# Performance work log

Hardware: AMD Instinct MI355X
Metric: run time of the kernel (lower is better)

Reference implementation:

```python
import jax, jax.numpy as jnp
import numpy as np

D_MODEL = 1024
NUM_HEADS = 16
D_K = D_MODEL // NUM_HEADS
BATCH = 4
SEQ = 2048


def setup_inputs() -> dict:
    key = jax.random.key(0)
    ks = jax.random.split(key, 16)
    s = 0.02
    return {
        "query": jax.random.normal(ks[0], (BATCH, SEQ, D_MODEL), jnp.float32),
        "key": jax.random.normal(ks[1], (BATCH, SEQ, D_MODEL), jnp.float32),
        "value": jax.random.normal(ks[2], (BATCH, SEQ, D_MODEL), jnp.float32),
        "Wq": jax.random.normal(ks[3], (D_MODEL, D_MODEL), jnp.float32) * s,
        "bq": jnp.zeros((D_MODEL,), jnp.float32),
        "Wk": jax.random.normal(ks[4], (D_MODEL, D_MODEL), jnp.float32) * s,
        "bk": jnp.zeros((D_MODEL,), jnp.float32),
        "Wv": jax.random.normal(ks[5], (D_MODEL, D_MODEL), jnp.float32) * s,
        "bv": jnp.zeros((D_MODEL,), jnp.float32),
        "Wo": jax.random.normal(ks[6], (D_MODEL, D_MODEL), jnp.float32) * s,
        "bo": jnp.zeros((D_MODEL,), jnp.float32),
        "gamma": jnp.ones((D_MODEL,), jnp.float32),
        "beta": jnp.zeros((D_MODEL,), jnp.float32),
    }


def _layer_norm(x, gamma, beta, eps=1e-5):
    mu = jnp.mean(x, axis=-1, keepdims=True)
    var = jnp.var(x, axis=-1, keepdims=True)
    return (x - mu) * jax.lax.rsqrt(var + eps) * gamma + beta


def reference(query, key, value, Wq, bq, Wk, bk, Wv, bv, Wo, bo, gamma, beta):
    B, S, _ = query.shape
    residual = query
    # projections -> [B, H, S, d_k]
    Q = (query @ Wq + bq).reshape(B, S, NUM_HEADS, D_K).transpose(0, 2, 1, 3)
    K = (key @ Wk + bk).reshape(B, -1, NUM_HEADS, D_K).transpose(0, 2, 1, 3)
    V = (value @ Wv + bv).reshape(B, -1, NUM_HEADS, D_K).transpose(0, 2, 1, 3)
    scale = 1.0 / jnp.sqrt(jnp.asarray(D_K, query.dtype))
    scores = jnp.einsum("bhqd,bhkd->bhqk", Q, K) * scale  # [B,H,S,S]
    attn = jax.nn.softmax(scores, axis=-1)
    ctx = jnp.einsum("bhqk,bhkd->bhqd", attn, V)
    ctx = ctx.transpose(0, 2, 1, 3).reshape(B, S, D_MODEL)
    out = ctx @ Wo + bo
    return _layer_norm(residual + out, gamma, beta)
```

## Files before the change

kernel.cpp:

```cpp
#include <hip/hip_runtime.h>

#define D_MODEL 1024
#define NUM_HEADS 16
#define DK 64
#define BATCH 4
#define SEQ 2048
#define MTOT (BATCH*SEQ)

typedef __attribute__((ext_vector_type(8))) short short8;
typedef __attribute__((ext_vector_type(4))) float f32x4;
typedef __attribute__((ext_vector_type(4))) unsigned int u32x4;

__device__ __forceinline__ unsigned short f2bf(float f) {
    union { float f; unsigned u; } v; v.f = f;
    unsigned r = v.u + 0x7FFFu + ((v.u >> 16) & 1u);
    return (unsigned short)(r >> 16);
}

__device__ __forceinline__ unsigned cvtpk(float lo, float hi) {
    unsigned r;
    asm("v_cvt_pk_bf16_f32 %0, %1, %2" : "=v"(r) : "v"(lo), "v"(hi));
    return r;
}

__device__ __forceinline__ void gload16(const unsigned short* g, unsigned short* l) {
    __builtin_amdgcn_global_load_lds(
        (const __attribute__((address_space(1))) unsigned int*)g,
        (__attribute__((address_space(3))) unsigned int*)l, 16, 0, 0);
}

__global__ __launch_bounds__(256) void mha_wtrans4(
    const float* __restrict__ W0, const float* __restrict__ W1,
    const float* __restrict__ W2, const float* __restrict__ W3,
    unsigned short* __restrict__ T0, unsigned short* __restrict__ T1,
    unsigned short* __restrict__ T2, unsigned short* __restrict__ T3) {
    __shared__ float tile[64][65];
    int z = blockIdx.z;
    const float* W = z == 0 ? W0 : z == 1 ? W1 : z == 2 ? W2 : W3;
    unsigned short* WT = z == 0 ? T0 : z == 1 ? T1 : z == 2 ? T2 : T3;
    int n0 = blockIdx.x * 64, k0 = blockIdx.y * 64;
    int tx = threadIdx.x & 63, ty = threadIdx.x >> 6;
#pragma unroll
    for (int i = 0; i < 16; ++i)
        tile[ty + i * 4][tx] = W[(size_t)(k0 + ty + i * 4) * D_MODEL + n0 + tx];
    __syncthreads();
#pragma unroll
    for (int i = 0; i < 16; ++i)
        WT[(size_t)(n0 + ty + i * 4) * D_MODEL + k0 + tx] = f2bf(tile[tx][ty + i * 4]);
}

__global__ __launch_bounds__(256) void mha_cvt3(
    const float* __restrict__ i0, const float* __restrict__ i1, const float* __restrict__ i2,
    unsigned short* __restrict__ o0, unsigned short* __restrict__ o1, unsigned short* __restrict__ o2) {
    int y = blockIdx.y;
    const float* in = y == 0 ? i0 : y == 1 ? i1 : i2;
    unsigned short* out = y == 0 ? o0 : y == 1 ? o1 : o2;
    int i = blockIdx.x * 256 + threadIdx.x;
    float4 v = reinterpret_cast<const float4*>(in)[i];
    ushort4 o;
    o.x = f2bf(v.x); o.y = f2bf(v.y); o.z = f2bf(v.z); o.w = f2bf(v.w);
    reinterpret_cast<ushort4*>(out)[i] = o;
}

__device__ __forceinline__ void gemm_stage(const unsigned short* Ag, const unsigned short* Bg,
                                           unsigned short* Al, unsigned short* Bl,
                                           int wid, int rsub, int c8, int kk,
                                           int brow, int bcol) {
#pragma unroll
    for (int q = 0; q < 4; ++q) {
        int i = wid * 4 + q;
        int row = i * 8 + rsub;
        int gcol = kk + ((c8 ^ (row & 7)) << 3);
        gload16(Ag + (size_t)(brow + row) * D_MODEL + gcol, Al + i * 512);
        gload16(Bg + (size_t)(bcol + row) * D_MODEL + gcol, Bl + i * 512);
    }
}

__device__ __forceinline__ void gemm_compute(const unsigned short* Al, const unsigned short* Bl,
                                             f32x4 (&acc)[4][4],
                                             int wr, int wc, int l15, int lg, int l7) {
    short8 af[4][2], bf[4][2];
#pragma unroll
    for (int mi = 0; mi < 4; ++mi)
#pragma unroll
        for (int ks = 0; ks < 2; ++ks)
            af[mi][ks] = *reinterpret_cast<const short8*>(
                &Al[(wr * 64 + mi * 16 + l15) * 64 + (((ks * 4 + lg) ^ l7) << 3)]);
#pragma unroll
    for (int ni = 0; ni < 4; ++ni)
#pragma unroll
        for (int ks = 0; ks < 2; ++ks)
            bf[ni][ks] = *reinterpret_cast<const short8*>(
                &Bl[(wc * 64 + ni * 16 + l15) * 64 + (((ks * 4 + lg) ^ l7) << 3)]);
#pragma unroll
    for (int mi = 0; mi < 4; ++mi)
#pragma unroll
        for (int ni = 0; ni < 4; ++ni)
#pragma unroll
            for (int ks = 0; ks < 2; ++ks)
                acc[mi][ni] = __builtin_amdgcn_mfma_f32_16x16x32_bf16(
                    af[mi][ks], bf[ni][ks], acc[mi][ni], 0, 0, 0);
}

__global__ __launch_bounds__(256) void mha_gemm_qkv(
    const unsigned short* __restrict__ Aq, const unsigned short* __restrict__ Ak,
    const unsigned short* __restrict__ Av,
    const unsigned short* __restrict__ Wq, const unsigned short* __restrict__ Wk,
    const unsigned short* __restrict__ Wv,
    const float* __restrict__ bq, const float* __restrict__ bk, const float* __restrict__ bv,
    unsigned short* __restrict__ Qb, unsigned short* __restrict__ Kb,
    unsigned short* __restrict__ VT, float qscale) {
    __shared__ unsigned short SM[32768];
    unsigned short* A0 = SM;
    unsigned short* B0 = SM + 8192;
    unsigned short* A1 = SM + 16384;
    unsigned short* B1 = SM + 24576;

    int z = blockIdx.z;
    const unsigned short* A = z == 0 ? Aq : z == 1 ? Ak : Av;
    const unsigned short* WT = z == 0 ? Wq : z == 1 ? Wk : Wv;
    const float* bias = z == 0 ? bq : z == 1 ? bk : bv;

    int wid = threadIdx.x >> 6;
    int lane = threadIdx.x & 63;
    int wr = wid >> 1, wc = wid & 1;
    int brow = blockIdx.x * 128;
    int bcol = blockIdx.y * 128;
    int l15 = lane & 15, lg = lane >> 4;
    int c8 = lane & 7, rsub = lane >> 3;
    int l7 = l15 & 7;

    f32x4 acc[4][4] = {};
    gemm_stage(A, WT, A0, B0, wid, rsub, c8, 0, brow, bcol);
    __syncthreads();
    for (int kk = 0; kk < D_MODEL; kk += 128) {
        gemm_stage(A, WT, A1, B1, wid, rsub, c8, kk + 64, brow, bcol);
        gemm_compute(A0, B0, acc, wr, wc, l15, lg, l7);
        __syncthreads();
        if (kk + 128 < D_MODEL)
            gemm_stage(A, WT, A0, B0, wid, rsub, c8, kk + 128, brow, bcol);
        gemm_compute(A1, B1, acc, wr, wc, l15, lg, l7);
        __syncthreads();
    }

    if (z < 2) {
        unsigned short* outb = z == 0 ? Qb : Kb;
        float scale = z == 0 ? qscale : 1.0f;
#pragma unroll
        for (int ni = 0; ni < 4; ++ni) {
            int col = bcol + wc * 64 + ni * 16 + l15;
            float bv2 = bias[col];
#pragma unroll
            for (int mi = 0; mi < 4; ++mi)
#pragma unroll
                for (int j = 0; j < 4; ++j) {
                    int row = brow + wr * 64 + mi * 16 + lg * 4 + j;
                    outb[(size_t)row * D_MODEL + col] = f2bf((acc[mi][ni][j] + bv2) * scale);
                }
        }
    } else {
        unsigned short* T = SM;
#pragma unroll
        for (int ni = 0; ni < 4; ++ni) {
            int c = wc * 64 + ni * 16 + l15;
            float bv2 = bias[bcol + c];
#pragma unroll
            for (int mi = 0; mi < 4; ++mi)
#pragma unroll
                for (int j = 0; j < 4; ++j) {
                    int r = wr * 64 + mi * 16 + lg * 4 + j;
                    T[c * 136 + r] = f2bf(acc[mi][ni][j] + bv2);
                }
        }
        __syncthreads();
        int c = threadIdx.x >> 1;
        int rh = (threadIdx.x & 1) * 64;
        int gcol = bcol + c;
        int h = gcol >> 6, d = gcol & 63;
        int b = brow >> 11, s0 = brow & (SEQ - 1);
        unsigned short* dst = VT + ((size_t)((b * 16 + h) * 64 + d)) * SEQ + s0 + rh;
        const unsigned short* src = &T[c * 136 + rh];
#pragma unroll
        for (int i = 0; i < 8; ++i)
            *reinterpret_cast<short8*>(dst + i * 8) =
                *reinterpret_cast<const short8*>(src + i * 8);
    }
}

__global__ __launch_bounds__(256) void mha_gemm_o(const unsigned short* __restrict__ A,
                                                  const unsigned short* __restrict__ WT,
                                                  const float* __restrict__ bias,
                                                  const float* __restrict__ residual,
                                                  float* __restrict__ outf) {
    __shared__ unsigned short SM[32768];
    unsigned short* A0 = SM;
    unsigned short* B0 = SM + 8192;
    unsigned short* A1 = SM + 16384;
    unsigned short* B1 = SM + 24576;

    int wid = threadIdx.x >> 6;
    int lane = threadIdx.x & 63;
    int wr = wid >> 1, wc = wid & 1;
    int brow = blockIdx.x * 128;
    int bcol = blockIdx.y * 128;
    int l15 = lane & 15, lg = lane >> 4;
    int c8 = lane & 7, rsub = lane >> 3;
    int l7 = l15 & 7;

    f32x4 acc[4][4] = {};
    gemm_stage(A, WT, A0, B0, wid, rsub, c8, 0, brow, bcol);
    __syncthreads();
    for (int kk = 0; kk < D_MODEL; kk += 128) {
        gemm_stage(A, WT, A1, B1, wid, rsub, c8, kk + 64, brow, bcol);
        gemm_compute(A0, B0, acc, wr, wc, l15, lg, l7);
        __syncthreads();
        if (kk + 128 < D_MODEL)
            gemm_stage(A, WT, A0, B0, wid, rsub, c8, kk + 128, brow, bcol);
        gemm_compute(A1, B1, acc, wr, wc, l15, lg, l7);
        __syncthreads();
    }
#pragma unroll
    for (int ni = 0; ni < 4; ++ni) {
        int col = bcol + wc * 64 + ni * 16 + l15;
        float bv2 = bias[col];
#pragma unroll
        for (int mi = 0; mi < 4; ++mi)
#pragma unroll
            for (int j = 0; j < 4; ++j) {
                int row = brow + wr * 64 + mi * 16 + lg * 4 + j;
                outf[(size_t)row * D_MODEL + col] =
                    acc[mi][ni][j] + bv2 + residual[(size_t)row * D_MODEL + col];
            }
    }
}

__device__ __forceinline__ void attn_tile(const unsigned short* Kd,
                                          const unsigned short* Vd,
                                          const short8 aq[2][2],
                                          f32x4 (&acc)[2][4],
                                          float (&lsum)[2],
                                          int l15, int lg, int l7) {
    f32x4 z[2][4];
#pragma unroll
    for (int t = 0; t < 4; ++t) {
        int krow = (t * 16 + l15) * 64;
        short8 kf0 = *reinterpret_cast<const short8*>(&Kd[krow + ((lg ^ l7) << 3)]);
        short8 kf1 = *reinterpret_cast<const short8*>(&Kd[krow + (((4 + lg) ^ l7) << 3)]);
#pragma unroll
        for (int m = 0; m < 2; ++m) {
            f32x4 zz = {};
            zz = __builtin_amdgcn_mfma_f32_16x16x32_bf16(kf0, aq[m][0], zz, 0, 0, 0);
            zz = __builtin_amdgcn_mfma_f32_16x16x32_bf16(kf1, aq[m][1], zz, 0, 0, 0);
            z[m][t] = zz;
        }
    }
#pragma unroll
    for (int m = 0; m < 2; ++m)
#pragma unroll
        for (int t = 0; t < 4; ++t)
#pragma unroll
            for (int j = 0; j < 4; ++j) {
                float p = __builtin_amdgcn_exp2f(z[m][t][j]);
                z[m][t][j] = p;
                lsum[m] += p;
            }
    short8 pf[2][2];
#pragma unroll
    for (int m = 0; m < 2; ++m)
#pragma unroll
        for (int ks = 0; ks < 2; ++ks) {
            union { u32x4 u; short8 s; } cv;
            cv.u = (u32x4){cvtpk(z[m][2 * ks][0], z[m][2 * ks][1]),
                           cvtpk(z[m][2 * ks][2], z[m][2 * ks][3]),
                           cvtpk(z[m][2 * ks + 1][0], z[m][2 * ks + 1][1]),
                           cvtpk(z[m][2 * ks + 1][2], z[m][2 * ks + 1][3])};
            pf[m][ks] = cv.s;
        }
#pragma unroll
    for (int dt = 0; dt < 4; ++dt) {
        int vrow = (dt * 16 + l15) * 64;
        short8 vf0 = *reinterpret_cast<const short8*>(&Vd[vrow + ((lg ^ l7) << 3)]);
        short8 vf1 = *reinterpret_cast<const short8*>(&Vd[vrow + (((4 + lg) ^ l7) << 3)]);
#pragma unroll
        for (int m = 0; m < 2; ++m) {
            acc[m][dt] = __builtin_amdgcn_mfma_f32_16x16x32_bf16(vf0, pf[m][0], acc[m][dt], 0, 0, 0);
            acc[m][dt] = __builtin_amdgcn_mfma_f32_16x16x32_bf16(vf1, pf[m][1], acc[m][dt], 0, 0, 0);
        }
    }
}

__global__ __launch_bounds__(256, 4) void mha_attn(const unsigned short* __restrict__ Q,
                                                   const unsigned short* __restrict__ K,
                                                   const unsigned short* __restrict__ VT,
                                                   unsigned short* __restrict__ ctx) {
    __shared__ unsigned short K0[64 * 64], V0[64 * 64];
    __shared__ unsigned short K1[64 * 64], V1[64 * 64];

    int lane = threadIdx.x & 63;
    int w = threadIdx.x >> 6;
    int l15 = lane & 15, lg = lane >> 4;
    int l7 = l15 & 7;
    int c8 = lane & 7, rsub = lane >> 3;

    int id = blockIdx.x + gridDim.x * blockIdx.y;
    int nid = (id & 7) * 128 + (id >> 3);
    int bx = nid & 15;
    int bh = nid >> 4;
    int b = bh >> 4, h = bh & 15;
    int q0 = bx * 128 + w * 32;

    short8 aq[2][2];
    {
        const unsigned short* Qp = Q + (size_t)(b * SEQ + q0) * D_MODEL + h * DK;
#pragma unroll
        for (int m = 0; m < 2; ++m)
#pragma unroll
            for (int ks = 0; ks < 2; ++ks)
                aq[m][ks] = *reinterpret_cast<const short8*>(
                    Qp + (size_t)(m * 16 + l15) * D_MODEL + ks * 32 + lg * 8);
    }

    f32x4 acc[2][4] = {};
    float lsum[2] = {};

    const unsigned short* Kbh = K + (size_t)(b * SEQ) * D_MODEL + h * DK;
    const unsigned short* VTbh = VT + (size_t)bh * DK * SEQ;

    int i0 = w * 2, i1 = w * 2 + 1;
    int row0 = i0 * 8 + rsub, row1 = i1 * 8 + rsub;
    int sw0 = (c8 ^ (row0 & 7)) << 3, sw1 = (c8 ^ (row1 & 7)) << 3;
    int sr0 = (row0 & 32) | ((row0 & 12) << 1) | ((row0 & 16) >> 2) | (row0 & 3);
    int sr1 = (row1 & 32) | ((row1 & 12) << 1) | ((row1 & 16) >> 2) | (row1 & 3);

#define STAGE(Kd, Vd, kb)                                                        \
    do {                                                                         \
        gload16(Kbh + (size_t)((kb) + sr0) * D_MODEL + sw0, (Kd) + i0 * 512);    \
        gload16(Kbh + (size_t)((kb) + sr1) * D_MODEL + sw1, (Kd) + i1 * 512);    \
        gload16(VTbh + (size_t)row0 * SEQ + (kb) + sw0, (Vd) + i0 * 512);        \
        gload16(VTbh + (size_t)row1 * SEQ + (kb) + sw1, (Vd) + i1 * 512);        \
    } while (0)

    STAGE(K0, V0, 0);
    __syncthreads();

    for (int kb = 0; kb < SEQ; kb += 128) {
        STAGE(K1, V1, kb + 64);
        attn_tile(K0, V0, aq, acc, lsum, l15, lg, l7);
        __syncthreads();
        if (kb + 128 < SEQ) STAGE(K0, V0, kb + 128);
        attn_tile(K1, V1, aq, acc, lsum, l15, lg, l7);
        __syncthreads();
    }
#undef STAGE

#pragma unroll
    for (int m = 0; m < 2; ++m) {
        float l = lsum[m];
        l += __shfl_xor(l, 16);
        l += __shfl_xor(l, 32);
        float rl = 1.0f / l;
        int q = q0 + m * 16 + l15;
        unsigned short* cp = ctx + (size_t)(b * SEQ + q) * D_MODEL + h * DK + lg * 4;
#pragma unroll
        for (int dt = 0; dt < 4; ++dt) {
            ushort4 o;
            o.x = f2bf(acc[m][dt][0] * rl);
            o.y = f2bf(acc[m][dt][1] * rl);
            o.z = f2bf(acc[m][dt][2] * rl);
            o.w = f2bf(acc[m][dt][3] * rl);
            *reinterpret_cast<ushort4*>(cp + dt * 16) = o;
        }
    }
}

__global__ __launch_bounds__(256) void mha_ln(const float* __restrict__ X,
                                              const float* __restrict__ gamma,
                                              const float* __restrict__ beta,
                                              float* __restrict__ out) {
    int row = blockIdx.x;
    int t = threadIdx.x;
    const float* x = X + (size_t)row * D_MODEL;
    float4 v = reinterpret_cast<const float4*>(x)[t];
    float s = v.x + v.y + v.z + v.w;
    float s2 = v.x * v.x + v.y * v.y + v.z * v.z + v.w * v.w;
#pragma unroll
    for (int off = 1; off < 64; off <<= 1) {
        s += __shfl_xor(s, off);
        s2 += __shfl_xor(s2, off);
    }
    __shared__ float ws[8];
    int wid = t >> 6;
    if ((t & 63) == 0) { ws[wid] = s; ws[4 + wid] = s2; }
    __syncthreads();
    s = ws[0] + ws[1] + ws[2] + ws[3];
    s2 = ws[4] + ws[5] + ws[6] + ws[7];
    float mu = s * (1.f / D_MODEL);
    float var = s2 * (1.f / D_MODEL) - mu * mu;
    float rstd = rsqrtf(var + 1e-5f);
    float4 gv = reinterpret_cast<const float4*>(gamma)[t];
    float4 bv = reinterpret_cast<const float4*>(beta)[t];
    float4 o;
    o.x = (v.x - mu) * rstd * gv.x + bv.x;
    o.y = (v.y - mu) * rstd * gv.y + bv.y;
    o.z = (v.z - mu) * rstd * gv.z + bv.z;
    o.w = (v.w - mu) * rstd * gv.w + bv.w;
    reinterpret_cast<float4*>(out + (size_t)row * D_MODEL)[t] = o;
}

extern "C" void kernel_launch(void* const* d_in, const int* in_sizes, int n_in,
                              void* d_out, int out_size, void* d_ws, size_t ws_size,
                              hipStream_t stream) {
    const float* query = (const float*)d_in[0];
    const float* key   = (const float*)d_in[1];
    const float* value = (const float*)d_in[2];
    const float* Wq = (const float*)d_in[3];
    const float* bq = (const float*)d_in[4];
    const float* Wk = (const float*)d_in[5];
    const float* bk = (const float*)d_in[6];
    const float* Wv = (const float*)d_in[7];
    const float* bv = (const float*)d_in[8];
    const float* Wo = (const float*)d_in[9];
    const float* bo = (const float*)d_in[10];
    const float* gamma = (const float*)d_in[11];
    const float* beta  = (const float*)d_in[12];

    char* ws = (char*)d_ws;
    const size_t MB = 1u << 20;
    unsigned short* WTq = (unsigned short*)(ws + 0 * MB);
    unsigned short* WTk = (unsigned short*)(ws + 2 * MB);
    unsigned short* WTv = (unsigned short*)(ws + 4 * MB);
    unsigned short* WTo = (unsigned short*)(ws + 6 * MB);
    unsigned short* Aq  = (unsigned short*)(ws + 8 * MB);
    unsigned short* Ak  = (unsigned short*)(ws + 24 * MB);
    unsigned short* Av  = (unsigned short*)(ws + 40 * MB);
    unsigned short* Qb  = (unsigned short*)(ws + 56 * MB);
    unsigned short* Kb  = (unsigned short*)(ws + 72 * MB);
    unsigned short* VT  = (unsigned short*)(ws + 88 * MB);
    unsigned short* ctx = (unsigned short*)(ws + 92 * MB);
    float* tmp          = (float*)(ws + 24 * MB);

    const float C1 = 0.180336880f;

    dim3 b256(256);
    mha_wtrans4<<<dim3(16, 16, 4), b256, 0, stream>>>(Wq, Wk, Wv, Wo, WTq, WTk, WTv, WTo);

    int nblk = (MTOT * D_MODEL / 4) / 256;
    mha_cvt3<<<dim3(nblk, 3), b256, 0, stream>>>(query, key, value, Aq, Ak, Av);

    mha_gemm_qkv<<<dim3(MTOT / 128, D_MODEL / 128, 3), b256, 0, stream>>>(
        Aq, Ak, Av, WTq, WTk, WTv, bq, bk, bv, Qb, Kb, VT, C1);

    mha_attn<<<dim3(SEQ / 128, BATCH * NUM_HEADS), b256, 0, stream>>>(Qb, Kb, VT, ctx);

    mha_gemm_o<<<dim3(MTOT / 128, D_MODEL / 128), b256, 0, stream>>>(ctx, WTo, bo, query, tmp);

    mha_ln<<<dim3(MTOT), b256, 0, stream>>>(tmp, gamma, beta, (float*)d_out);
}
```

Measured before the change: 200.2 us.

## Single-buffer GEMMs, split QKV projection per input, enlarge attention query tile

The projection and output GEMMs drop LDS double buffering for a single 64-wide K stage with two barriers per step. The fused QKV launch becomes three per-input convert+GEMM pairs that reuse one bf16 staging buffer. Attention now gives each wave 64 queries instead of 32 (256 per block), which halves K/V tile reloads per query but raises register pressure, so the occupancy launch bound was removed. The trade-off is less load/compute overlap in the GEMMs and more serialized launches, in exchange for smaller LDS and workspace footprint.

Result: slower. 236.7 us (+18.3%).

```diff
diff --git a/kernel.cpp b/kernel.cpp
--- a/kernel.cpp
+++ b/kernel.cpp
@@ -49,12 +49,8 @@
         WT[(size_t)(n0 + ty + i * 4) * D_MODEL + k0 + tx] = f2bf(tile[tx][ty + i * 4]);
 }
 
-__global__ __launch_bounds__(256) void mha_cvt3(
-    const float* __restrict__ i0, const float* __restrict__ i1, const float* __restrict__ i2,
-    unsigned short* __restrict__ o0, unsigned short* __restrict__ o1, unsigned short* __restrict__ o2) {
-    int y = blockIdx.y;
-    const float* in = y == 0 ? i0 : y == 1 ? i1 : i2;
-    unsigned short* out = y == 0 ? o0 : y == 1 ? o1 : o2;
+__global__ __launch_bounds__(256) void mha_cvt(const float* __restrict__ in,
+                                               unsigned short* __restrict__ out) {
     int i = blockIdx.x * 256 + threadIdx.x;
     float4 v = reinterpret_cast<const float4*>(in)[i];
     ushort4 o;
@@ -102,24 +98,14 @@
                     af[mi][ks], bf[ni][ks], acc[mi][ni], 0, 0, 0);
 }
 
-__global__ __launch_bounds__(256) void mha_gemm_qkv(
-    const unsigned short* __restrict__ Aq, const unsigned short* __restrict__ Ak,
-    const unsigned short* __restrict__ Av,
-    const unsigned short* __restrict__ Wq, const unsigned short* __restrict__ Wk,
-    const unsigned short* __restrict__ Wv,
-    const float* __restrict__ bq, const float* __restrict__ bk, const float* __restrict__ bv,
-    unsigned short* __restrict__ Qb, unsigned short* __restrict__ Kb,
-    unsigned short* __restrict__ VT, float qscale) {
-    __shared__ unsigned short SM[32768];
-    unsigned short* A0 = SM;
-    unsigned short* B0 = SM + 8192;
-    unsigned short* A1 = SM + 16384;
-    unsigned short* B1 = SM + 24576;
-
-    int z = blockIdx.z;
-    const unsigned short* A = z == 0 ? Aq : z == 1 ? Ak : Av;
-    const unsigned short* WT = z == 0 ? Wq : z == 1 ? Wk : Wv;
-    const float* bias = z == 0 ? bq : z == 1 ? bk : bv;
+template <int MODE>
+__global__ __launch_bounds__(256) void mha_gemm_proj(
+    const unsigned short* __restrict__ A, const unsigned short* __restrict__ WT,
+    const float* __restrict__ bias,
+    unsigned short* __restrict__ outb, unsigned short* __restrict__ VT, float scale) {
+    __shared__ unsigned short SM[MODE == 2 ? 17408 : 16384];
+    unsigned short* Al = SM;
+    unsigned short* Bl = SM + 8192;
 
     int wid = threadIdx.x >> 6;
     int lane = threadIdx.x & 63;
@@ -131,21 +117,14 @@
     int l7 = l15 & 7;
 
     f32x4 acc[4][4] = {};
-    gemm_stage(A, WT, A0, B0, wid, rsub, c8, 0, brow, bcol);
-    __syncthreads();
-    for (int kk = 0; kk < D_MODEL; kk += 128) {
-        gemm_stage(A, WT, A1, B1, wid, rsub, c8, kk + 64, brow, bcol);
-        gemm_compute(A0, B0, acc, wr, wc, l15, lg, l7);
-        __syncthreads();
-        if (kk + 128 < D_MODEL)
-            gemm_stage(A, WT, A0, B0, wid, rsub, c8, kk + 128, brow, bcol);
-        gemm_compute(A1, B1, acc, wr, wc, l15, lg, l7);
-        __syncthreads();
-    }
-
-    if (z < 2) {
-        unsigned short* outb = z == 0 ? Qb : Kb;
-        float scale = z == 0 ? qscale : 1.0f;
+    for (int kk = 0; kk < D_MODEL; kk += 64) {
+        __syncthreads();
+        gemm_stage(A, WT, Al, Bl, wid, rsub, c8, kk, brow, bcol);
+        __syncthreads();
+        gemm_compute(Al, Bl, acc, wr, wc, l15, lg, l7);
+    }
+
+    if (MODE == 0) {
 #pragma unroll
         for (int ni = 0; ni < 4; ++ni) {
             int col = bcol + wc * 64 + ni * 16 + l15;
@@ -159,6 +138,7 @@
                 }
         }
     } else {
+        __syncthreads();
         unsigned short* T = SM;
 #pragma unroll
         for (int ni = 0; ni < 4; ++ni) {
@@ -192,11 +172,9 @@
                                                   const float* __restrict__ bias,
                                                   const float* __restrict__ residual,
                                                   float* __restrict__ outf) {
-    __shared__ unsigned short SM[32768];
-    unsigned short* A0 = SM;
-    unsigned short* B0 = SM + 8192;
-    unsigned short* A1 = SM + 16384;
-    unsigned short* B1 = SM + 24576;
+    __shared__ unsigned short SM[16384];
+    unsigned short* Al = SM;
+    unsigned short* Bl = SM + 8192;
 
     int wid = threadIdx.x >> 6;
     int lane = threadIdx.x & 63;
@@ -208,16 +186,11 @@
     int l7 = l15 & 7;
 
     f32x4 acc[4][4] = {};
-    gemm_stage(A, WT, A0, B0, wid, rsub, c8, 0, brow, bcol);
-    __syncthreads();
-    for (int kk = 0; kk < D_MODEL; kk += 128) {
-        gemm_stage(A, WT, A1, B1, wid, rsub, c8, kk + 64, brow, bcol);
-        gemm_compute(A0, B0, acc, wr, wc, l15, lg, l7);
-        __syncthreads();
-        if (kk + 128 < D_MODEL)
-            gemm_stage(A, WT, A0, B0, wid, rsub, c8, kk + 128, brow, bcol);
-        gemm_compute(A1, B1, acc, wr, wc, l15, lg, l7);
-        __syncthreads();
+    for (int kk = 0; kk < D_MODEL; kk += 64) {
+        __syncthreads();
+        gemm_stage(A, WT, Al, Bl, wid, rsub, c8, kk, brow, bcol);
+        __syncthreads();
+        gemm_compute(Al, Bl, acc, wr, wc, l15, lg, l7);
     }
 #pragma unroll
     for (int ni = 0; ni < 4; ++ni) {
@@ -234,20 +207,20 @@
     }
 }
 
-__device__ __forceinline__ void attn_tile(const unsigned short* Kd,
-                                          const unsigned short* Vd,
-                                          const short8 aq[2][2],
-                                          f32x4 (&acc)[2][4],
-                                          float (&lsum)[2],
-                                          int l15, int lg, int l7) {
-    f32x4 z[2][4];
+__device__ __forceinline__ void attn_tile4(const unsigned short* Kd,
+                                           const unsigned short* Vd,
+                                           const short8 (&aq)[4][2],
+                                           f32x4 (&acc)[4][4],
+                                           float (&lsum)[4],
+                                           int l15, int lg, int l7) {
+    f32x4 z[4][4];
 #pragma unroll
     for (int t = 0; t < 4; ++t) {
         int krow = (t * 16 + l15) * 64;
         short8 kf0 = *reinterpret_cast<const short8*>(&Kd[krow + ((lg ^ l7) << 3)]);
         short8 kf1 = *reinterpret_cast<const short8*>(&Kd[krow + (((4 + lg) ^ l7) << 3)]);
 #pragma unroll
-        for (int m = 0; m < 2; ++m) {
+        for (int m = 0; m < 4; ++m) {
             f32x4 zz = {};
             zz = __builtin_amdgcn_mfma_f32_16x16x32_bf16(kf0, aq[m][0], zz, 0, 0, 0);
             zz = __builtin_amdgcn_mfma_f32_16x16x32_bf16(kf1, aq[m][1], zz, 0, 0, 0);
@@ -255,7 +228,7 @@
         }
     }
 #pragma unroll
-    for (int m = 0; m < 2; ++m)
+    for (int m = 0; m < 4; ++m)
 #pragma unroll
         for (int t = 0; t < 4; ++t)
 #pragma unroll
@@ -264,9 +237,9 @@
                 z[m][t][j] = p;
                 lsum[m] += p;
             }
-    short8 pf[2][2];
-#pragma unroll
-    for (int m = 0; m < 2; ++m)
+    short8 pf[4][2];
+#pragma unroll
+    for (int m = 0; m < 4; ++m)
 #pragma unroll
         for (int ks = 0; ks < 2; ++ks) {
             union { u32x4 u; short8 s; } cv;
@@ -282,17 +255,17 @@
         short8 vf0 = *reinterpret_cast<const short8*>(&Vd[vrow + ((lg ^ l7) << 3)]);
         short8 vf1 = *reinterpret_cast<const short8*>(&Vd[vrow + (((4 + lg) ^ l7) << 3)]);
 #pragma unroll
-        for (int m = 0; m < 2; ++m) {
+        for (int m = 0; m < 4; ++m) {
             acc[m][dt] = __builtin_amdgcn_mfma_f32_16x16x32_bf16(vf0, pf[m][0], acc[m][dt], 0, 0, 0);
             acc[m][dt] = __builtin_amdgcn_mfma_f32_16x16x32_bf16(vf1, pf[m][1], acc[m][dt], 0, 0, 0);
         }
     }
 }
 
-__global__ __launch_bounds__(256, 4) void mha_attn(const unsigned short* __restrict__ Q,
-                                                   const unsigned short* __restrict__ K,
-                                                   const unsigned short* __restrict__ VT,
-                                                   unsigned short* __restrict__ ctx) {
+__global__ __launch_bounds__(256) void mha_attn(const unsigned short* __restrict__ Q,
+                                                const unsigned short* __restrict__ K,
+                                                const unsigned short* __restrict__ VT,
+                                                unsigned short* __restrict__ ctx) {
     __shared__ unsigned short K0[64 * 64], V0[64 * 64];
     __shared__ unsigned short K1[64 * 64], V1[64 * 64];
 
@@ -302,26 +275,26 @@
     int l7 = l15 & 7;
     int c8 = lane & 7, rsub = lane >> 3;
 
-    int id = blockIdx.x + gridDim.x * blockIdx.y;
-    int nid = (id & 7) * 128 + (id >> 3);
-    int bx = nid & 15;
-    int bh = nid >> 4;
+    int id = blockIdx.x;
+    int nid = (id & 7) * 64 + (id >> 3);
+    int bx = nid & 7;
+    int bh = nid >> 3;
     int b = bh >> 4, h = bh & 15;
-    int q0 = bx * 128 + w * 32;
-
-    short8 aq[2][2];
+    int q0 = bx * 256 + w * 64;
+
+    short8 aq[4][2];
     {
         const unsigned short* Qp = Q + (size_t)(b * SEQ + q0) * D_MODEL + h * DK;
 #pragma unroll
-        for (int m = 0; m < 2; ++m)
+        for (int m = 0; m < 4; ++m)
 #pragma unroll
             for (int ks = 0; ks < 2; ++ks)
                 aq[m][ks] = *reinterpret_cast<const short8*>(
                     Qp + (size_t)(m * 16 + l15) * D_MODEL + ks * 32 + lg * 8);
     }
 
-    f32x4 acc[2][4] = {};
-    float lsum[2] = {};
+    f32x4 acc[4][4] = {};
+    float lsum[4] = {};
 
     const unsigned short* Kbh = K + (size_t)(b * SEQ) * D_MODEL + h * DK;
     const unsigned short* VTbh = VT + (size_t)bh * DK * SEQ;
@@ -345,16 +318,16 @@
 
     for (int kb = 0; kb < SEQ; kb += 128) {
         STAGE(K1, V1, kb + 64);
-        attn_tile(K0, V0, aq, acc, lsum, l15, lg, l7);
+        attn_tile4(K0, V0, aq, acc, lsum, l15, lg, l7);
         __syncthreads();
         if (kb + 128 < SEQ) STAGE(K0, V0, kb + 128);
-        attn_tile(K1, V1, aq, acc, lsum, l15, lg, l7);
+        attn_tile4(K1, V1, aq, acc, lsum, l15, lg, l7);
         __syncthreads();
     }
 #undef STAGE
 
 #pragma unroll
-    for (int m = 0; m < 2; ++m) {
+    for (int m = 0; m < 4; ++m) {
         float l = lsum[m];
         l += __shfl_xor(l, 16);
         l += __shfl_xor(l, 32);
@@ -430,29 +403,33 @@
     unsigned short* WTk = (unsigned short*)(ws + 2 * MB);
     unsigned short* WTv = (unsigned short*)(ws + 4 * MB);
     unsigned short* WTo = (unsigned short*)(ws + 6 * MB);
-    unsigned short* Aq  = (unsigned short*)(ws + 8 * MB);
-    unsigned short* Ak  = (unsigned short*)(ws + 24 * MB);
-    unsigned short* Av  = (unsigned short*)(ws + 40 * MB);
-    unsigned short* Qb  = (unsigned short*)(ws + 56 * MB);
-    unsigned short* Kb  = (unsigned short*)(ws + 72 * MB);
-    unsigned short* VT  = (unsigned short*)(ws + 88 * MB);
-    unsigned short* ctx = (unsigned short*)(ws + 92 * MB);
-    float* tmp          = (float*)(ws + 24 * MB);
+    unsigned short* Ab  = (unsigned short*)(ws + 8 * MB);
+    unsigned short* Qb  = (unsigned short*)(ws + 25 * MB);
+    unsigned short* Kb  = (unsigned short*)(ws + 42 * MB);
+    unsigned short* VT  = (unsigned short*)(ws + 59 * MB);
+    unsigned short* ctx = (unsigned short*)(ws + 76 * MB);
+    float* tmp          = (float*)(ws + 8 * MB);
 
     const float C1 = 0.180336880f;
 
     dim3 b256(256);
+    dim3 ggrid(MTOT / 128, D_MODEL / 128);
+    int nblk = (MTOT * D_MODEL / 4) / 256;
+
     mha_wtrans4<<<dim3(16, 16, 4), b256, 0, stream>>>(Wq, Wk, Wv, Wo, WTq, WTk, WTv, WTo);
 
-    int nblk = (MTOT * D_MODEL / 4) / 256;
-    mha_cvt3<<<dim3(nblk, 3), b256, 0, stream>>>(query, key, value, Aq, Ak, Av);
-
-    mha_gemm_qkv<<<dim3(MTOT / 128, D_MODEL / 128, 3), b256, 0, stream>>>(
-        Aq, Ak, Av, WTq, WTk, WTv, bq, bk, bv, Qb, Kb, VT, C1);
-
-    mha_attn<<<dim3(SEQ / 128, BATCH * NUM_HEADS), b256, 0, stream>>>(Qb, Kb, VT, ctx);
-
-    mha_gemm_o<<<dim3(MTOT / 128, D_MODEL / 128), b256, 0, stream>>>(ctx, WTo, bo, query, tmp);
+    mha_cvt<<<dim3(nblk), b256, 0, stream>>>(query, Ab);
+    mha_gemm_proj<0><<<ggrid, b256, 0, stream>>>(Ab, WTq, bq, Qb, nullptr, C1);
+
+    mha_cvt<<<dim3(nblk), b256, 0, stream>>>(key, Ab);
+    mha_gemm_proj<0><<<ggrid, b256, 0, stream>>>(Ab, WTk, bk, Kb, nullptr, 1.0f);
+
+    mha_cvt<<<dim3(nblk), b256, 0, stream>>>(value, Ab);
+    mha_gemm_proj<2><<<ggrid, b256, 0, stream>>>(Ab, WTv, bv, nullptr, VT, 1.0f);
+
+    mha_attn<<<dim3(BATCH * NUM_HEADS * SEQ / 256), b256, 0, stream>>>(Qb, Kb, VT, ctx);
+
+    mha_gemm_o<<<ggrid, b256, 0, stream>>>(ctx, WTo, bo, query, tmp);
 
     mha_ln<<<dim3(MTOT), b256, 0, stream>>>(tmp, gamma, beta, (float*)d_out);
 }
```
